# Performance work log

Hardware: AMD Instinct MI355X
Metric: run time of the kernel (lower is better)

Reference implementation:

```python
import jax, jax.numpy as jnp
import numpy as np

BS, M, N = 256, 128, 1024
ITERS = 100
ALPHA = 0.1


def setup_inputs() -> dict:
    key = jax.random.key(0)
    k1, k2, k3, k4 = jax.random.split(key, 4)
    A = jax.random.normal(k1, (BS, M, N), dtype=jnp.float32)
    b = jax.random.normal(k2, (BS, M), dtype=jnp.float32)
    D1 = jax.random.normal(k3, (BS, N), dtype=jnp.float32)
    D2 = jax.random.normal(k4, (BS, N), dtype=jnp.float32)
    return {"A": A, "b": b, "D1": D1, "D2": D2, "bs": BS}


def _soft_thresholding(x, alpha, D1, D2):
    t = alpha * jnp.abs(D1)
    denom = 1.0 + 2.0 * alpha * D2 ** 2
    return jnp.where(x - t > 0, (x - t) / denom,
                     jnp.where(x + t < 0, (x + t) / denom, jnp.zeros_like(x)))


def reference(A, b, D1, D2, bs):
    n = D1.shape[1]
    # A is loop-invariant, so AAT^{-1} is identical every iteration; hoist it.
    AAT = jnp.einsum('bmn,bkn->bmk', A, A)          # (bs, m, m)
    AAT_inv = jnp.linalg.inv(AAT)

    def projection(y):
        Ay_minus_b = jnp.einsum('bmn,bn->bm', A, y) - b
        u = jnp.einsum('bmk,bk->bm', AAT_inv, Ay_minus_b)
        correction = jnp.einsum('bmn,bm->bn', A, u)  # A^T u
        return y - correction

    def step(carry, _):
        x, z = carry
        x_half = _soft_thresholding(z, ALPHA, D1, D2)
        x_new = projection(2.0 * x_half - z)
        z_new = z + x_new - x_half
        return (x_new, z_new), None

    x0 = jnp.zeros((bs, n), dtype=jnp.float32)
    z0 = jnp.zeros((bs, n), dtype=jnp.float32)
    (x, _), _ = jax.lax.scan(step, (x0, z0), None, length=ITERS)
    return x
```

## Files before the change

### kernel.cpp

```cpp
#include <hip/hip_runtime.h>
#include <math.h>

#define BS 256
#define MM 128
#define NN 1024
#define ITERS 100
#define ALPHA 0.1f
#define AST 129
#define IST 129
#define TRP 132

typedef _Float16 half8 __attribute__((ext_vector_type(8)));
typedef _Float16 half4 __attribute__((ext_vector_type(4)));
typedef _Float16 half2v __attribute__((ext_vector_type(2)));
typedef float f32x4 __attribute__((ext_vector_type(4)));

template <int CTRL>
__device__ __forceinline__ float dpp_add(float x) {
  int xi = __builtin_bit_cast(int, x);
  int r = __builtin_amdgcn_update_dpp(xi, xi, CTRL, 0xf, 0xf, true);
  return x + __builtin_bit_cast(float, r);
}

__global__ __attribute__((amdgpu_waves_per_eu(4, 4)))
__launch_bounds__(1024) void k_fused(
    const float* __restrict__ A, const float* __restrict__ bvec,
    const float* __restrict__ D1, const float* __restrict__ D2,
    float* __restrict__ out, _Float16* __restrict__ ATh) {
  union BigU {
    struct {
      float As[64 * AST];
      __align__(16) _Float16 Thi[8][2][64][8];
      __align__(16) _Float16 Tlo[8][2][64][8];
      float Msh[MM * IST];
    } p1;
    __align__(16) _Float16 AL[512 * MM];
  };
  __shared__ BigU bu;
  __shared__ float2 tdi_sh[NN];
  __shared__ float b_sh[MM];
  __shared__ __align__(16) _Float16 s_h[MM];
  __shared__ __align__(16) _Float16 u_h[MM];
  __shared__ __align__(16) float t_redW[32][TRP];
  __shared__ float fcol[2][MM];
  __shared__ float frow[2][MM];

  int b = blockIdx.x;
  int tid = threadIdx.x;
  const float* Ab = A + (size_t)b * MM * NN;
  _Float16* ATb = ATh + (size_t)b * NN * MM;

  {
    float* As = bu.p1.As;
    auto& Thi = bu.p1.Thi;
    auto& Tlo = bu.p1.Tlo;
    int lane = tid & 63;
    int w16 = tid >> 6;
    int wr = w16 & 3;
    int wc = w16 >> 2;
    f32x4 acc[2][2];
#pragma unroll
    for (int i = 0; i < 2; ++i)
#pragma unroll
      for (int jj = 0; jj < 2; ++jj) acc[i][jj] = (f32x4){0.f, 0.f, 0.f, 0.f};

    for (int t = 0; t < 16; ++t) {
      int k0 = t * 64;
#pragma unroll
      for (int s = 0; s < 2; ++s) {
        int c = tid + 1024 * s;
        int m = c >> 4;
        int q = c & 15;
        int kl = q * 4;
        float4 v = *(const float4*)&Ab[(size_t)m * NN + k0 + kl];
        As[(kl + 0) * AST + m] = v.x;
        As[(kl + 1) * AST + m] = v.y;
        As[(kl + 2) * AST + m] = v.z;
        As[(kl + 3) * AST + m] = v.w;
        _Float16 h0 = (_Float16)v.x, h1 = (_Float16)v.y;
        _Float16 h2 = (_Float16)v.z, h3 = (_Float16)v.w;
        half4 hv = {h0, h1, h2, h3};
        half4 lv = {(_Float16)(v.x - (float)h0), (_Float16)(v.y - (float)h1),
                    (_Float16)(v.z - (float)h2), (_Float16)(v.w - (float)h3)};
        int strip = m >> 4;
        int kc = kl >> 5;
        int ln = (m & 15) + (((kl & 31) >> 3) << 4);
        int j0 = kl & 7;
        *(half4*)&Thi[strip][kc][ln][j0] = hv;
        *(half4*)&Tlo[strip][kc][ln][j0] = lv;
      }
      __syncthreads();
#pragma unroll
      for (int s = 0; s < 4; ++s) {
        int idx = tid + 1024 * s;
        int nl = idx >> 6;
        int mp = idx & 63;
        half2v hv;
        hv[0] = (_Float16)As[nl * AST + 2 * mp];
        hv[1] = (_Float16)As[nl * AST + 2 * mp + 1];
        *(half2v*)&ATb[(size_t)(k0 + nl) * MM + 2 * mp] = hv;
      }
#pragma unroll
      for (int kc = 0; kc < 2; ++kc) {
        half8 ahi[2], alo[2], bhi[2], blo[2];
#pragma unroll
        for (int i = 0; i < 2; ++i) {
          ahi[i] = *(const half8*)&Thi[2 * wr + i][kc][lane][0];
          alo[i] = *(const half8*)&Tlo[2 * wr + i][kc][lane][0];
          bhi[i] = *(const half8*)&Thi[2 * wc + i][kc][lane][0];
          blo[i] = *(const half8*)&Tlo[2 * wc + i][kc][lane][0];
        }
#pragma unroll
        for (int i = 0; i < 2; ++i)
#pragma unroll
          for (int jj = 0; jj < 2; ++jj) {
            acc[i][jj] = __builtin_amdgcn_mfma_f32_16x16x32_f16(
                ahi[i], bhi[jj], acc[i][jj], 0, 0, 0);
            acc[i][jj] = __builtin_amdgcn_mfma_f32_16x16x32_f16(
                ahi[i], blo[jj], acc[i][jj], 0, 0, 0);
            acc[i][jj] = __builtin_amdgcn_mfma_f32_16x16x32_f16(
                alo[i], bhi[jj], acc[i][jj], 0, 0, 0);
          }
      }
      __syncthreads();
    }
    float* Msh = bu.p1.Msh;
    int rbase = 4 * (lane >> 4), cbase = lane & 15;
#pragma unroll
    for (int i = 0; i < 2; ++i)
#pragma unroll
      for (int jj = 0; jj < 2; ++jj) {
        int r0 = (2 * wr + i) * 16 + rbase;
        int c0 = (2 * wc + jj) * 16 + cbase;
#pragma unroll
        for (int r_ = 0; r_ < 4; ++r_)
          Msh[(r0 + r_) * IST + c0] = acc[i][jj][r_];
      }
  }
  __syncthreads();

  {
    float* Msh = bu.p1.Msh;
    int j = tid & 127;
    int i0 = (tid >> 7) * 16;
    float m[16];
#pragma unroll
    for (int ii = 0; ii < 16; ++ii) m[ii] = Msh[(i0 + ii) * IST + j];
    if (tid < MM) {
      fcol[0][tid] = Msh[tid * IST];
      frow[0][tid] = Msh[tid];
    }
    __syncthreads();
    int cur = 0;
    for (int kb = 0; kb < 8; ++kb) {
#pragma unroll
      for (int kq = 0; kq < 16; ++kq) {
        int k = kb * 16 + kq;
        float p = 1.0f / fcol[cur][k];
        float mkj = frow[cur][j];
        float fik[16];
#pragma unroll
        for (int ii = 0; ii < 16; ++ii) fik[ii] = fcol[cur][i0 + ii];
        float pmkj = p * mkj;
        bool pivslab = (i0 == kb * 16);
        if (j == k) {
#pragma unroll
          for (int ii = 0; ii < 16; ++ii) m[ii] = -p * fik[ii];
          if (pivslab) m[kq] = p;
        } else {
#pragma unroll
          for (int ii = 0; ii < 16; ++ii) m[ii] = fmaf(-fik[ii], pmkj, m[ii]);
          if (pivslab) m[kq] = pmkj;
        }
        int nxt = cur ^ 1;
        if (k < MM - 1) {
          if (j == k + 1) {
#pragma unroll
            for (int ii = 0; ii < 16; ++ii) fcol[nxt][i0 + ii] = m[ii];
          }
          if (i0 == ((k + 1) & ~15)) frow[nxt][j] = m[(kq + 1) & 15];
        }
        __syncthreads();
        cur = nxt;
      }
    }
#pragma unroll
    for (int ii = 0; ii < 16; ++ii) Msh[(i0 + ii) * IST + j] = m[ii];
  }
  __syncthreads();

  int sub = tid & 7, rrow = tid >> 3;
  float ghf[8];
  {
    const float* Msh = bu.p1.Msh;
#pragma unroll
    for (int s = 0; s < 4; ++s) {
      int base = rrow * IST + 16 * sub + 4 * s;
      float v0 = Msh[base + 0], v1 = Msh[base + 1];
      float v2 = Msh[base + 2], v3 = Msh[base + 3];
      half2v h0; h0[0] = (_Float16)v0; h0[1] = (_Float16)v1;
      half2v h1; h1[0] = (_Float16)v2; h1[1] = (_Float16)v3;
      ghf[2 * s + 0] = __builtin_bit_cast(float, h0);
      ghf[2 * s + 1] = __builtin_bit_cast(float, h1);
    }
  }
#pragma unroll
  for (int s = 0; s < 8; ++s) asm volatile("" : "+v"(ghf[s]));
  __syncthreads();

  _Float16* AL = bu.AL;
  {
    float d1 = D1[(size_t)b * NN + tid];
    float d2 = D2[(size_t)b * NN + tid];
    float2 td2;
    td2.x = ALPHA * fabsf(d1);
    td2.y = 1.0f / (1.0f + 2.0f * ALPHA * d2 * d2);
    tdi_sh[tid] = td2;
  }
  if (tid < MM) {
    float bb = bvec[(size_t)b * MM + tid];
    b_sh[tid] = bb;
    s_h[tid] = (_Float16)(-bb);
  }

  int l8 = tid & 7;
  int g = (tid >> 3) & 7;
  int w = tid >> 6;
  int mb = 16 * l8;
  int alsw = (g & 1) * 8;

#pragma unroll
  for (int i = 0; i < 8; ++i) {
    int c = tid + 1024 * i;
    int col = c >> 4;
    int m8 = (c & 15) * 8;
    int n = 32 * (col >> 5) + 32 + col;
    int phys = m8 ^ ((col & 1) << 3);
    *(half8*)&AL[col * MM + phys] = *(const half8*)&ATb[(size_t)n * MM + m8];
  }

  float rcw[16];
  {
    int n0 = 64 * w + 16 + g, n1 = 64 * w + 24 + g;
    f32x4 v0 = *(const f32x4*)&ATb[(size_t)n0 * MM + mb];
    f32x4 v1 = *(const f32x4*)&ATb[(size_t)n0 * MM + mb + 8];
    f32x4 v2 = *(const f32x4*)&ATb[(size_t)n1 * MM + mb];
    f32x4 v3 = *(const f32x4*)&ATb[(size_t)n1 * MM + mb + 8];
    rcw[0] = v0[0]; rcw[1] = v0[1]; rcw[2] = v0[2]; rcw[3] = v0[3];
    rcw[4] = v1[0]; rcw[5] = v1[1]; rcw[6] = v1[2]; rcw[7] = v1[3];
    rcw[8] = v2[0]; rcw[9] = v2[1]; rcw[10] = v2[2]; rcw[11] = v2[3];
    rcw[12] = v3[0]; rcw[13] = v3[1]; rcw[14] = v3[2]; rcw[15] = v3[3];
  }
#pragma unroll
  for (int k = 0; k < 16; ++k) asm volatile("" : "+v"(rcw[k]));

  float zz[8];
#pragma unroll
  for (int k = 0; k < 8; ++k) zz[k] = 0.0f;

  __syncthreads();

  for (int it = 0; it < ITERS; ++it) {
    bool last = (it == ITERS - 1);

    f32x4 sa0 = *(const f32x4*)&ATb[(size_t)(64 * w + g) * MM + mb];
    f32x4 sa1 = *(const f32x4*)&ATb[(size_t)(64 * w + g) * MM + mb + 8];
    f32x4 sb0 = *(const f32x4*)&ATb[(size_t)(64 * w + 8 + g) * MM + mb];
    f32x4 sb1 = *(const f32x4*)&ATb[(size_t)(64 * w + 8 + g) * MM + mb + 8];

    {
      int j0 = 16 * sub;
      half8 sA = *(const half8*)&s_h[j0];
      half8 sB = *(const half8*)&s_h[j0 + 8];
      float up = 0.0f;
      up = __builtin_amdgcn_fdot2(__builtin_bit_cast(half2v, ghf[0]),
                                  __builtin_shufflevector(sA, sA, 0, 1), up, false);
      up = __builtin_amdgcn_fdot2(__builtin_bit_cast(half2v, ghf[1]),
                                  __builtin_shufflevector(sA, sA, 2, 3), up, false);
      up = __builtin_amdgcn_fdot2(__builtin_bit_cast(half2v, ghf[2]),
                                  __builtin_shufflevector(sA, sA, 4, 5), up, false);
      up = __builtin_amdgcn_fdot2(__builtin_bit_cast(half2v, ghf[3]),
                                  __builtin_shufflevector(sA, sA, 6, 7), up, false);
      up = __builtin_amdgcn_fdot2(__builtin_bit_cast(half2v, ghf[4]),
                                  __builtin_shufflevector(sB, sB, 0, 1), up, false);
      up = __builtin_amdgcn_fdot2(__builtin_bit_cast(half2v, ghf[5]),
                                  __builtin_shufflevector(sB, sB, 2, 3), up, false);
      up = __builtin_amdgcn_fdot2(__builtin_bit_cast(half2v, ghf[6]),
                                  __builtin_shufflevector(sB, sB, 4, 5), up, false);
      up = __builtin_amdgcn_fdot2(__builtin_bit_cast(half2v, ghf[7]),
                                  __builtin_shufflevector(sB, sB, 6, 7), up, false);
      up = dpp_add<0xB1>(up);
      up = dpp_add<0x4E>(up);
      up = dpp_add<0x141>(up);
      if (sub == 0) u_h[rrow] = (_Float16)up;
    }
    __syncthreads();
    half8 uA = *(const half8*)&u_h[mb];
    half8 uB = *(const half8*)&u_h[mb + 8];
    half2v u0 = __builtin_shufflevector(uA, uA, 0, 1);
    half2v u1 = __builtin_shufflevector(uA, uA, 2, 3);
    half2v u2 = __builtin_shufflevector(uA, uA, 4, 5);
    half2v u3 = __builtin_shufflevector(uA, uA, 6, 7);
    half2v u4 = __builtin_shufflevector(uB, uB, 0, 1);
    half2v u5 = __builtin_shufflevector(uB, uB, 2, 3);
    half2v u6 = __builtin_shufflevector(uB, uB, 4, 5);
    half2v u7 = __builtin_shufflevector(uB, uB, 6, 7);

    float t[16];
#pragma unroll
    for (int k = 0; k < 16; ++k) t[k] = 0.0f;

    auto colstep = [&](half8 ha, half8 hb, int n, float zv) -> float {
      float cp = 0.0f;
      cp = __builtin_amdgcn_fdot2(__builtin_shufflevector(ha, ha, 0, 1), u0, cp, false);
      cp = __builtin_amdgcn_fdot2(__builtin_shufflevector(ha, ha, 2, 3), u1, cp, false);
      cp = __builtin_amdgcn_fdot2(__builtin_shufflevector(ha, ha, 4, 5), u2, cp, false);
      cp = __builtin_amdgcn_fdot2(__builtin_shufflevector(ha, ha, 6, 7), u3, cp, false);
      cp = __builtin_amdgcn_fdot2(__builtin_shufflevector(hb, hb, 0, 1), u4, cp, false);
      cp = __builtin_amdgcn_fdot2(__builtin_shufflevector(hb, hb, 2, 3), u5, cp, false);
      cp = __builtin_amdgcn_fdot2(__builtin_shufflevector(hb, hb, 4, 5), u6, cp, false);
      cp = __builtin_amdgcn_fdot2(__builtin_shufflevector(hb, hb, 6, 7), u7, cp, false);
      cp = dpp_add<0xB1>(cp);
      cp = dpp_add<0x4E>(cp);
      cp = dpp_add<0x141>(cp);
      float2 tdi = tdi_sh[n];
      float td = tdi.x, di = tdi.y;
      float xm = zv - td, xp = zv + td;
      float xh = xm > 0.0f ? xm * di : (xp < 0.0f ? xp * di : 0.0f);
      if (!last) {
        float z1 = xh - cp;
        float xm1 = z1 - td, xp1 = z1 + td;
        float xh1 = xm1 > 0.0f ? xm1 * di : (xp1 < 0.0f ? xp1 * di : 0.0f);
        float y = 2.0f * xh1 - z1;
        f32x4 wa = __builtin_bit_cast(f32x4, ha);
        f32x4 wb = __builtin_bit_cast(f32x4, hb);
#pragma unroll
        for (int i2 = 0; i2 < 4; ++i2) {
          asm("v_fma_mix_f32 %0, %1, %2, %0 op_sel_hi:[1,0,0]"
              : "+v"(t[2 * i2]) : "v"(wa[i2]), "v"(y));
          asm("v_fma_mix_f32 %0, %1, %2, %0 op_sel:[1,0,0] op_sel_hi:[1,0,0]"
              : "+v"(t[2 * i2 + 1]) : "v"(wa[i2]), "v"(y));
          asm("v_fma_mix_f32 %0, %1, %2, %0 op_sel_hi:[1,0,0]"
              : "+v"(t[8 + 2 * i2]) : "v"(wb[i2]), "v"(y));
          asm("v_fma_mix_f32 %0, %1, %2, %0 op_sel:[1,0,0] op_sel_hi:[1,0,0]"
              : "+v"(t[8 + 2 * i2 + 1]) : "v"(wb[i2]), "v"(y));
        }
        return z1;
      } else {
        float y = 2.0f * xh - zv;
        if (l8 == 0) out[(size_t)b * NN + n] = y - cp;
        return zv;
      }
    };

    {
      f32x4 ra = {rcw[0], rcw[1], rcw[2], rcw[3]};
      f32x4 rb = {rcw[4], rcw[5], rcw[6], rcw[7]};
      zz[0] = colstep(__builtin_bit_cast(half8, ra),
                      __builtin_bit_cast(half8, rb), 64 * w + 16 + g, zz[0]);
      f32x4 rc_ = {rcw[8], rcw[9], rcw[10], rcw[11]};
      f32x4 rd_ = {rcw[12], rcw[13], rcw[14], rcw[15]};
      zz[1] = colstep(__builtin_bit_cast(half8, rc_),
                      __builtin_bit_cast(half8, rd_), 64 * w + 24 + g, zz[1]);
    }
#pragma unroll
    for (int j = 0; j < 4; ++j) {
      const _Float16* ap = &AL[(32 * w + 8 * j + g) * MM];
      half8 ha = *(const half8*)&ap[mb + alsw];
      half8 hb = *(const half8*)&ap[mb + 8 - alsw];
      zz[2 + j] = colstep(ha, hb, 64 * w + 32 + 8 * j + g, zz[2 + j]);
    }
    zz[6] = colstep(__builtin_bit_cast(half8, sa0),
                    __builtin_bit_cast(half8, sa1), 64 * w + g, zz[6]);
    zz[7] = colstep(__builtin_bit_cast(half8, sb0),
                    __builtin_bit_cast(half8, sb1), 64 * w + 8 + g, zz[7]);

    if (!last) {
#pragma unroll
      for (int k = 0; k < 16; ++k) {
        t[k] = dpp_add<0x128>(t[k]);
        t[k] += __shfl_xor(t[k], 32);
      }
      if ((g & 5) == 0) {
        int row = 2 * w + (g >> 1);
#pragma unroll
        for (int s2 = 0; s2 < 4; ++s2) {
          f32x4 tv = {t[4 * s2], t[4 * s2 + 1], t[4 * s2 + 2], t[4 * s2 + 3]};
          *(f32x4*)&t_redW[row][mb + 4 * s2] = tv;
        }
      }
      __syncthreads();
      if (tid < MM) {
        float ssum = -b_sh[tid];
#pragma unroll
        for (int h = 0; h < 32; ++h) ssum += t_redW[h][tid];
        s_h[tid] = (_Float16)ssum;
      }
      __syncthreads();
    }
  }
}

extern "C" void kernel_launch(void* const* d_in, const int* in_sizes, int n_in,
                              void* d_out, int out_size, void* d_ws, size_t ws_size,
                              hipStream_t stream) {
  const float* A  = (const float*)d_in[0];
  const float* bv = (const float*)d_in[1];
  const float* D1 = (const float*)d_in[2];
  const float* D2 = (const float*)d_in[3];
  float* out = (float*)d_out;

  _Float16* ATh = (_Float16*)d_ws;

  k_fused<<<BS, 1024, 0, stream>>>(A, bv, D1, D2, out, ATh);
}
```

Baseline: 727.4 us.

## Split fused kernel into prep and main kernels, prefetch next A tile

The single fused kernel is split into a prep kernel (Gram matrix via split-fp16 MFMA, inversion, writing fp16 transposed A and the fp16 inverse to workspace) and a main kernel that reads both back and runs the iterations. The prep loop now issues the global loads for the next 64-column tile of A right after staging the current one, so their latency can hide behind the MFMA work. Splitting frees the shared-memory union, so each kernel's LDS layout is independent. The cost is an extra launch and a global round trip for the inverse matrix.

```diff
diff --git a/kernel.cpp b/kernel.cpp
--- a/kernel.cpp
+++ b/kernel.cpp
@@ -23,25 +23,13 @@
 }
 
 __global__ __attribute__((amdgpu_waves_per_eu(4, 4)))
-__launch_bounds__(1024) void k_fused(
-    const float* __restrict__ A, const float* __restrict__ bvec,
-    const float* __restrict__ D1, const float* __restrict__ D2,
-    float* __restrict__ out, _Float16* __restrict__ ATh) {
-  union BigU {
-    struct {
-      float As[64 * AST];
-      __align__(16) _Float16 Thi[8][2][64][8];
-      __align__(16) _Float16 Tlo[8][2][64][8];
-      float Msh[MM * IST];
-    } p1;
-    __align__(16) _Float16 AL[512 * MM];
-  };
-  __shared__ BigU bu;
-  __shared__ float2 tdi_sh[NN];
-  __shared__ float b_sh[MM];
-  __shared__ __align__(16) _Float16 s_h[MM];
-  __shared__ __align__(16) _Float16 u_h[MM];
-  __shared__ __align__(16) float t_redW[32][TRP];
+__launch_bounds__(1024) void k_prep(const float* __restrict__ A,
+                                    _Float16* __restrict__ ATh,
+                                    _Float16* __restrict__ Gh) {
+  __shared__ float As[64 * AST];
+  __shared__ __align__(16) _Float16 Thi[8][2][64][8];
+  __shared__ __align__(16) _Float16 Tlo[8][2][64][8];
+  __shared__ float Msh[MM * IST];
   __shared__ float fcol[2][MM];
   __shared__ float frow[2][MM];
 
@@ -49,47 +37,56 @@
   int tid = threadIdx.x;
   const float* Ab = A + (size_t)b * MM * NN;
   _Float16* ATb = ATh + (size_t)b * NN * MM;
+  _Float16* Ghb = Gh + (size_t)b * MM * MM;
 
   {
-    float* As = bu.p1.As;
-    auto& Thi = bu.p1.Thi;
-    auto& Tlo = bu.p1.Tlo;
     int lane = tid & 63;
     int w16 = tid >> 6;
     int wr = w16 & 3;
     int wc = w16 >> 2;
+    int m0 = tid >> 4;
+    int m1 = m0 + 64;
+    int q0 = tid & 15;
+    int kl = q0 * 4;
+    int strip0 = m0 >> 4, strip1 = m1 >> 4;
+    int kc_s = kl >> 5;
+    int ln0 = (m0 & 15) + (((kl & 31) >> 3) << 4);
+    int ln1 = (m1 & 15) + (((kl & 31) >> 3) << 4);
+    int j0s = kl & 7;
+
     f32x4 acc[2][2];
 #pragma unroll
     for (int i = 0; i < 2; ++i)
 #pragma unroll
       for (int jj = 0; jj < 2; ++jj) acc[i][jj] = (f32x4){0.f, 0.f, 0.f, 0.f};
+
+    auto stage = [&](int m, int strip, int ln, float4 v) {
+      As[(kl + 0) * AST + m] = v.x;
+      As[(kl + 1) * AST + m] = v.y;
+      As[(kl + 2) * AST + m] = v.z;
+      As[(kl + 3) * AST + m] = v.w;
+      _Float16 h0 = (_Float16)v.x, h1 = (_Float16)v.y;
+      _Float16 h2 = (_Float16)v.z, h3 = (_Float16)v.w;
+      half4 hv = {h0, h1, h2, h3};
+      half4 lv = {(_Float16)(v.x - (float)h0), (_Float16)(v.y - (float)h1),
+                  (_Float16)(v.z - (float)h2), (_Float16)(v.w - (float)h3)};
+      *(half4*)&Thi[strip][kc_s][ln][j0s] = hv;
+      *(half4*)&Tlo[strip][kc_s][ln][j0s] = lv;
+    };
+
+    float4 va = *(const float4*)&Ab[(size_t)m0 * NN + kl];
+    float4 vb = *(const float4*)&Ab[(size_t)m1 * NN + kl];
 
     for (int t = 0; t < 16; ++t) {
       int k0 = t * 64;
-#pragma unroll
-      for (int s = 0; s < 2; ++s) {
-        int c = tid + 1024 * s;
-        int m = c >> 4;
-        int q = c & 15;
-        int kl = q * 4;
-        float4 v = *(const float4*)&Ab[(size_t)m * NN + k0 + kl];
-        As[(kl + 0) * AST + m] = v.x;
-        As[(kl + 1) * AST + m] = v.y;
-        As[(kl + 2) * AST + m] = v.z;
-        As[(kl + 3) * AST + m] = v.w;
-        _Float16 h0 = (_Float16)v.x, h1 = (_Float16)v.y;
-        _Float16 h2 = (_Float16)v.z, h3 = (_Float16)v.w;
-        half4 hv = {h0, h1, h2, h3};
-        half4 lv = {(_Float16)(v.x - (float)h0), (_Float16)(v.y - (float)h1),
-                    (_Float16)(v.z - (float)h2), (_Float16)(v.w - (float)h3)};
-        int strip = m >> 4;
-        int kc = kl >> 5;
-        int ln = (m & 15) + (((kl & 31) >> 3) << 4);
-        int j0 = kl & 7;
-        *(half4*)&Thi[strip][kc][ln][j0] = hv;
-        *(half4*)&Tlo[strip][kc][ln][j0] = lv;
-      }
+      stage(m0, strip0, ln0, va);
+      stage(m1, strip1, ln1, vb);
       __syncthreads();
+      if (t < 15) {
+        int k0n = k0 + 64;
+        va = *(const float4*)&Ab[(size_t)m0 * NN + k0n + kl];
+        vb = *(const float4*)&Ab[(size_t)m1 * NN + k0n + kl];
+      }
 #pragma unroll
       for (int s = 0; s < 4; ++s) {
         int idx = tid + 1024 * s;
@@ -124,7 +121,6 @@
       }
       __syncthreads();
     }
-    float* Msh = bu.p1.Msh;
     int rbase = 4 * (lane >> 4), cbase = lane & 15;
 #pragma unroll
     for (int i = 0; i < 2; ++i)
@@ -140,7 +136,6 @@
   __syncthreads();
 
   {
-    float* Msh = bu.p1.Msh;
     int j = tid & 127;
     int i0 = (tid >> 7) * 16;
     float m[16];
@@ -185,30 +180,43 @@
       }
     }
 #pragma unroll
-    for (int ii = 0; ii < 16; ++ii) Msh[(i0 + ii) * IST + j] = m[ii];
-  }
-  __syncthreads();
+    for (int ii = 0; ii < 16; ++ii)
+      Ghb[(size_t)(i0 + ii) * MM + j] = (_Float16)m[ii];
+  }
+}
+
+__global__ __attribute__((amdgpu_waves_per_eu(4, 4)))
+__launch_bounds__(1024) void k_main(
+    const _Float16* __restrict__ AT, const _Float16* __restrict__ Gh,
+    const float* __restrict__ bvec, const float* __restrict__ D1,
+    const float* __restrict__ D2, float* __restrict__ out) {
+  __shared__ __align__(16) _Float16 AL[512 * MM];
+  __shared__ float2 tdi_sh[NN];
+  __shared__ float b_sh[MM];
+  __shared__ __align__(16) _Float16 s_h[MM];
+  __shared__ __align__(16) _Float16 u_h[MM];
+  __shared__ __align__(16) float t_redW[32][TRP];
+
+  int b = blockIdx.x;
+  int tid = threadIdx.x;
+  const _Float16* ATb = AT + (size_t)b * NN * MM;
+  const _Float16* Ghb = Gh + (size_t)b * MM * MM;
 
   int sub = tid & 7, rrow = tid >> 3;
   float ghf[8];
   {
-    const float* Msh = bu.p1.Msh;
+    half8 g0 = *(const half8*)&Ghb[(size_t)rrow * MM + 16 * sub];
+    half8 g1 = *(const half8*)&Ghb[(size_t)rrow * MM + 16 * sub + 8];
+    f32x4 gA = __builtin_bit_cast(f32x4, g0);
+    f32x4 gB = __builtin_bit_cast(f32x4, g1);
 #pragma unroll
     for (int s = 0; s < 4; ++s) {
-      int base = rrow * IST + 16 * sub + 4 * s;
-      float v0 = Msh[base + 0], v1 = Msh[base + 1];
-      float v2 = Msh[base + 2], v3 = Msh[base + 3];
-      half2v h0; h0[0] = (_Float16)v0; h0[1] = (_Float16)v1;
-      half2v h1; h1[0] = (_Float16)v2; h1[1] = (_Float16)v3;
-      ghf[2 * s + 0] = __builtin_bit_cast(float, h0);
-      ghf[2 * s + 1] = __builtin_bit_cast(float, h1);
+      ghf[s] = gA[s];
+      ghf[4 + s] = gB[s];
     }
   }
 #pragma unroll
   for (int s = 0; s < 8; ++s) asm volatile("" : "+v"(ghf[s]));
-  __syncthreads();
-
-  _Float16* AL = bu.AL;
   {
     float d1 = D1[(size_t)b * NN + tid];
     float d2 = D2[(size_t)b * NN + tid];
@@ -411,6 +419,8 @@
   float* out = (float*)d_out;
 
   _Float16* ATh = (_Float16*)d_ws;
-
-  k_fused<<<BS, 1024, 0, stream>>>(A, bv, D1, D2, out, ATh);
+  _Float16* Gh = (_Float16*)((char*)d_ws + (size_t)BS * NN * MM * 2);
+
+  k_prep<<<BS, 1024, 0, stream>>>(A, ATh, Gh);
+  k_main<<<BS, 1024, 0, stream>>>(ATh, Gh, bv, D1, D2, out);
 }
```

Measured after the change: 713.7 us. Within noise of the previous version (-1.9%).
